# Optimization experiments

Measured on AMD Instinct MI355X. Metric: run time of the kernel, lower is better.

Reference implementation:

```python
import jax, jax.numpy as jnp
import numpy as np

H, HKV, DH, T_MAX = 32, 8, 128, 4096
ROPE_BASE = 500000.0


def apply_rope(x, pos, base):
    # x: [B, h, T, D]; MLX rope, traditional=False (split-half rotation)
    B, h, T, D = x.shape
    half = D // 2
    inv_freq = 1.0 / (base ** (jnp.arange(half, dtype=jnp.float32) * 2.0 / D))
    t = (pos + jnp.arange(T)).astype(jnp.float32)  # absolute positions
    ang = t[:, None] * inv_freq[None, :]           # [T, half]
    cos = jnp.cos(ang)[None, None]                 # [1,1,T,half]
    sin = jnp.sin(ang)[None, None]
    x1, x2 = x[..., :half], x[..., half:]
    return jnp.concatenate([x1 * cos - x2 * sin, x2 * cos + x1 * sin], axis=-1)


def setup_inputs() -> dict:
    key = jax.random.key(0)
    ks = jax.random.split(key, 5)
    hidden = 4096
    return {
        "hidden_states": jax.random.normal(ks[0], (1, 2048, hidden), jnp.float32),
        "Wq": jax.random.normal(ks[1], (hidden, H * DH), jnp.float32) * 0.02,
        "Wk": jax.random.normal(ks[2], (hidden, HKV * DH), jnp.float32) * 0.02,
        "Wv": jax.random.normal(ks[3], (hidden, HKV * DH), jnp.float32) * 0.02,
        "Wo": jax.random.normal(ks[4], (H * DH, hidden), jnp.float32) * 0.02,
        "pos_int": 0,
    }


def reference(hidden_states, Wq, Wk, Wv, Wo, pos_int):
    B, T, _ = hidden_states.shape
    q = (hidden_states @ Wq).reshape(B, T, H, DH).transpose(0, 2, 1, 3)    # [B,H,T,D]
    k = (hidden_states @ Wk).reshape(B, T, HKV, DH).transpose(0, 2, 1, 3)  # [B,Hkv,T,D]
    v = (hidden_states @ Wv).reshape(B, T, HKV, DH).transpose(0, 2, 1, 3)

    q = apply_rope(q, pos_int, ROPE_BASE)
    k = apply_rope(k, pos_int, ROPE_BASE)

    # KV cache: write at [pos:pos+T], then slice [:pos+T] (pos is static Python int)
    k_cache = jnp.zeros((B, HKV, T_MAX, DH), jnp.float32)
    v_cache = jnp.zeros((B, HKV, T_MAX, DH), jnp.float32)
    k_cache = jax.lax.dynamic_update_slice(k_cache, k, (0, 0, pos_int, 0))
    v_cache = jax.lax.dynamic_update_slice(v_cache, v, (0, 0, pos_int, 0))
    end_pos = pos_int + T
    k_ = k_cache[:, :, :end_pos, :]  # [B,Hkv,S,D]
    v_ = v_cache[:, :, :end_pos, :]
    S = end_pos

    # GQA without materializing repeat_interleave: group query heads per kv head
    group = H // HKV
    qg = q.reshape(B, HKV, group, T, DH)
    scale = 1.0 / jnp.sqrt(jnp.float32(DH))
    scores = jnp.einsum("bhgtd,bhsd->bhgts", qg, k_) * scale  # [B,Hkv,g,T,S]
    # torch SDPA is_causal=True: top-left aligned mask (allow s <= t)
    causal = jnp.arange(S)[None, :] <= jnp.arange(T)[:, None]  # [T,S]
    scores = jnp.where(causal[None, None, None], scores, -jnp.inf)
    probs = jax.nn.softmax(scores, axis=-1)
    attn = jnp.einsum("bhgts,bhsd->bhgtd", probs, v_)          # [B,Hkv,g,T,D]
    attn = attn.reshape(B, H, T, DH).transpose(0, 2, 1, 3).reshape(B, T, H * DH)
    return attn @ Wo
```

## Files before the change

kernel.cpp:

```cpp
#include <hip/hip_runtime.h>
#include <hip/hip_bf16.h>
#include <math.h>

typedef unsigned short u16;
typedef __attribute__((ext_vector_type(4))) float f32x4;
typedef __attribute__((ext_vector_type(8))) short bf16x8;

#define GLD16(gptr, lptr) __builtin_amdgcn_global_load_lds( \
    (const __attribute__((address_space(1))) void*)(gptr),  \
    (__attribute__((address_space(3))) void*)(lptr), 16, 0, 0)

__device__ __forceinline__ float bf2f(u16 u) {
  union { unsigned int i; float f; } c; c.i = ((unsigned int)u) << 16; return c.f;
}
__device__ __forceinline__ u16 f2bf(float f) {
  union { float f; unsigned int i; } c; c.f = f;
  unsigned int r = c.i + 0x7fffu + ((c.i >> 16) & 1u);
  return (u16)(r >> 16);
}

__global__ __launch_bounds__(256) void f32_to_bf16(const float* __restrict__ in,
                                                   u16* __restrict__ out, int n4) {
  int i = blockIdx.x * 256 + threadIdx.x;
  if (i >= n4) return;
  float4 v = reinterpret_cast<const float4*>(in)[i];
  ushort4 o;
  o.x = f2bf(v.x); o.y = f2bf(v.y); o.z = f2bf(v.z); o.w = f2bf(v.w);
  reinterpret_cast<ushort4*>(out)[i] = o;
}

__global__ __launch_bounds__(256) void transpose_qkv_w(const float* __restrict__ Wq,
                                                       const float* __restrict__ Wk,
                                                       const float* __restrict__ Wv,
                                                       u16* __restrict__ WT) {
  __shared__ float tile[32][33];
  const int bx = blockIdx.x, k0 = blockIdx.y * 32;
  const float* W; int n0, N; size_t outbase;
  if (bx < 128)      { W = Wq; n0 = bx * 32;          N = 4096; outbase = 0; }
  else if (bx < 160) { W = Wk; n0 = (bx - 128) * 32;  N = 1024; outbase = (size_t)4096 * 4096; }
  else               { W = Wv; n0 = (bx - 160) * 32;  N = 1024; outbase = (size_t)5120 * 4096; }
  const int tx = threadIdx.x & 31, ty = threadIdx.x >> 5;
#pragma unroll
  for (int r = 0; r < 32; r += 8)
    tile[ty + r][tx] = W[(size_t)(k0 + ty + r) * N + (n0 + tx)];
  __syncthreads();
#pragma unroll
  for (int r = 0; r < 32; r += 8)
    WT[outbase + (size_t)(n0 + ty + r) * 4096 + (k0 + tx)] = f2bf(tile[tx][ty + r]);
}

__global__ __launch_bounds__(256) void transpose_convert(const float* __restrict__ W,
                                                         u16* __restrict__ Wt,
                                                         int K, int N) {
  __shared__ float tile[32][33];
  const int n0 = blockIdx.x * 32, k0 = blockIdx.y * 32;
  const int tx = threadIdx.x & 31, ty = threadIdx.x >> 5;
#pragma unroll
  for (int r = 0; r < 32; r += 8)
    tile[ty + r][tx] = W[(size_t)(k0 + ty + r) * N + (n0 + tx)];
  __syncthreads();
#pragma unroll
  for (int r = 0; r < 32; r += 8)
    Wt[(size_t)(n0 + ty + r) * K + (k0 + tx)] = f2bf(tile[tx][ty + r]);
}

__global__ __launch_bounds__(256) void transpose_v(const u16* __restrict__ Vsrc,
                                                   u16* __restrict__ Vt) {
  __shared__ u16 tile[32][33];
  const int t0 = blockIdx.x * 32, d0 = blockIdx.y * 32, hkv = blockIdx.z;
  const int tx = threadIdx.x & 31, ty = threadIdx.x >> 5;
#pragma unroll
  for (int r = 0; r < 32; r += 8)
    tile[ty + r][tx] = Vsrc[(size_t)(t0 + ty + r) * 6144 + hkv * 128 + d0 + tx];
  __syncthreads();
#pragma unroll
  for (int r = 0; r < 32; r += 8)
    Vt[((size_t)hkv * 128 + d0 + ty + r) * 2048 + t0 + tx] = tile[tx][ty + r];
}

__global__ __launch_bounds__(256) void rope_table(float2* __restrict__ tab,
                                                  const int* __restrict__ pos_ptr) {
  int idx = blockIdx.x * 256 + threadIdx.x;
  int d = idx & 63, t = idx >> 6;
  int pos = *pos_ptr;
  float inv = exp2f(-(float)d * (0.015625f * 18.931568569324174f));
  float ang = (float)(pos + t) * inv;
  tab[idx] = make_float2(cosf(ang), sinf(ang));
}

__global__ __launch_bounds__(256) void rope_apply_qk(u16* __restrict__ QKV,
                                                     const float2* __restrict__ tab) {
  int idx = blockIdx.x * 256 + threadIdx.x;
  if (idx >= 2048 * 40 * 64) return;
  int d = idx & 63;
  int hh = (idx >> 6) % 40;
  int t = idx / (64 * 40);
  float2 cs = tab[t * 64 + d];
  const int col = (hh < 32) ? hh * 128 : 4096 + (hh - 32) * 128;
  size_t base = (size_t)t * 6144 + col + d;
  float x1 = bf2f(QKV[base]);
  float x2 = bf2f(QKV[base + 64]);
  QKV[base]      = f2bf(x1 * cs.x - x2 * cs.y);
  QKV[base + 64] = f2bf(x2 * cs.x + x1 * cs.y);
}

template <int BN, int OUT_BF16>
__global__ __launch_bounds__(512, 4) void gemm_2cu(const u16* __restrict__ A,
                                                   const u16* __restrict__ Bt,
                                                   void* __restrict__ C,
                                                   int M, int N, int K) {
  constexpr int NF = BN / 64;
  constexpr int WCOL = BN / 4;
  constexpr int LB = BN / 64;
  __shared__ alignas(16) u16 As[2][128 * 64];
  __shared__ alignas(16) u16 Bs[2][BN * 64];
  const int tid = threadIdx.x;
  const int lane = tid & 63, wid = tid >> 6;
  const int l15 = lane & 15, lg = lane >> 4;
  const int wm = wid >> 2, wn = wid & 3;
  const int wvb = tid & ~63;

  const int gy = gridDim.y;
  const int id0 = blockIdx.y * gridDim.x + blockIdx.x;
  const int xcd = id0 & 7;
  const int l = id0 >> 3;
  const int m0 = (l % gy) * 128;
  const int n0 = (xcd * (gridDim.x >> 3) + l / gy) * BN;

  f32x4 acc[4][NF];
#pragma unroll
  for (int i = 0; i < 4; ++i)
#pragma unroll
    for (int j = 0; j < NF; ++j) {
      f32x4 zz = {0.f, 0.f, 0.f, 0.f};
      acc[i][j] = zz;
    }

#define STAGE(s_, b_)                                                           \
  do {                                                                          \
    _Pragma("unroll")                                                           \
    for (int p = 0; p < 2; ++p) {                                               \
      const int slot = p * 512 + tid;                                           \
      const int row = slot >> 3, ch = slot & 7;                                 \
      const int col = (ch ^ (row & 7)) * 8;                                     \
      GLD16(A + (size_t)(m0 + row) * K + (s_) * 64 + col,                       \
            &As[b_][(p * 512 + wvb) * 8]);                                      \
    }                                                                           \
    _Pragma("unroll")                                                           \
    for (int p = 0; p < LB; ++p) {                                              \
      const int slot = p * 512 + tid;                                           \
      const int row = slot >> 3, ch = slot & 7;                                 \
      const int col = (ch ^ (row & 7)) * 8;                                     \
      GLD16(Bt + (size_t)(n0 + row) * K + (s_) * 64 + col,                      \
            &Bs[b_][(p * 512 + wvb) * 8]);                                      \
    }                                                                           \
  } while (0)

  STAGE(0, 0);
  __syncthreads();
  int cur = 0;

  const int nt = K >> 6;
  for (int t = 0; t < nt; ++t) {
    if (t + 1 < nt) STAGE(t + 1, cur ^ 1);
#pragma unroll
    for (int g = 0; g < 2; ++g) {
      bf16x8 af[4], bfr[NF];
#pragma unroll
      for (int i = 0; i < 4; ++i) {
        const int row = wm * 64 + i * 16 + l15;
        const int ch = (g * 4 + lg) ^ (row & 7);
        af[i] = *reinterpret_cast<const bf16x8*>(&As[cur][row * 64 + ch * 8]);
      }
#pragma unroll
      for (int j = 0; j < NF; ++j) {
        const int row = wn * WCOL + j * 16 + l15;
        const int ch = (g * 4 + lg) ^ (row & 7);
        bfr[j] = *reinterpret_cast<const bf16x8*>(&Bs[cur][row * 64 + ch * 8]);
      }
      __builtin_amdgcn_s_setprio(1);
#pragma unroll
      for (int i = 0; i < 4; ++i)
#pragma unroll
        for (int j = 0; j < NF; ++j)
          acc[i][j] = __builtin_amdgcn_mfma_f32_16x16x32_bf16(af[i], bfr[j], acc[i][j], 0, 0, 0);
      __builtin_amdgcn_s_setprio(0);
    }
    __syncthreads();
    cur ^= 1;
  }
#undef STAGE

#pragma unroll
  for (int i = 0; i < 4; ++i)
#pragma unroll
    for (int j = 0; j < NF; ++j)
#pragma unroll
      for (int r = 0; r < 4; ++r) {
        const int row = m0 + wm * 64 + i * 16 + lg * 4 + r;
        const int col = n0 + wn * WCOL + j * 16 + l15;
        const float v = acc[i][j][r];
        if (OUT_BF16) ((u16*)C)[(size_t)row * N + col] = f2bf(v);
        else          ((float*)C)[(size_t)row * N + col] = v;
      }
}

__global__ __launch_bounds__(512) void attn_kernel(const u16* __restrict__ Q,
                                                   const u16* __restrict__ K,
                                                   const u16* __restrict__ Vt,
                                                   u16* __restrict__ O,
                                                   const int* __restrict__ pos_ptr) {
  const int pos = *pos_ptr;
  const int id = (int)(blockIdx.y * gridDim.x + blockIdx.x);
  const int hkv = id & 7;
  const int h = hkv * 4 + ((id >> 3) & 3);
  const int qp = id >> 5;
  const int tid = threadIdx.x;
  const int w = tid >> 6, lane = tid & 63;
  const int l15 = lane & 15, lg = lane >> 4;

  __shared__ alignas(16) u16 Ks[2][64 * 128];
  __shared__ alignas(16) u16 Vs[2][128 * 64];
  __shared__ alignas(16) u16 Pl[8][16][72];

  const u16* Kh = K + hkv * 128;
  const u16* Vh = Vt + (size_t)hkv * 128 * 2048;

  const float C = 0.12752961957823275f;
  const float THR = 62.0f;
  const int wvb = tid & ~63;

#define STAGE_TILE(st_, b_)                                                        \
  do {                                                                             \
    const int s0_ = (st_) * 64;                                                    \
    _Pragma("unroll")                                                              \
    for (int p = 0; p < 2; ++p) {                                                  \
      const int idx = p * 512 + tid;                                               \
      const int kr = idx >> 4, kc = (idx & 15) ^ (kr & 7);                         \
      GLD16(Kh + (size_t)(s0_ + kr) * 6144 + kc * 8, &Ks[b_][(p * 512 + wvb) * 8]);\
      const int vr = idx >> 3, vc = (idx & 7) ^ (vr & 7);                          \
      GLD16(Vh + (size_t)vr * 2048 + s0_ + vc * 8, &Vs[b_][(p * 512 + wvb) * 8]);  \
    }                                                                              \
  } while (0)

  for (int pass = 0; pass < 2; ++pass) {
    const int qb = (pass == 0) ? (8 + qp) : (7 - qp);
    const int qt0 = qb * 128;
    const int nst = 2 * qb + 2;
    const int frag_base = qt0 + w * 16;

    bf16x8 qa[4];
#pragma unroll
    for (int kk = 0; kk < 4; ++kk)
      qa[kk] = *reinterpret_cast<const bf16x8*>(
          Q + (size_t)(frag_base + l15) * 6144 + h * 128 + kk * 32 + lg * 8);

    f32x4 acc[8];
#pragma unroll
    for (int i = 0; i < 8; ++i) { f32x4 z = {0.f, 0.f, 0.f, 0.f}; acc[i] = z; }
    float mrun[4], lpart[4];
#pragma unroll
    for (int r = 0; r < 4; ++r) {
      mrun[r] = (pos > 0) ? 0.0f : -INFINITY;
      lpart[r] = 0.0f;
    }

    STAGE_TILE(0, 0);
    __syncthreads();
    int cur = 0;

    for (int st = 0; st < nst; ++st) {
      if (st + 1 < nst) STAGE_TILE(st + 1, cur ^ 1);
      const int s0 = st * 64;

      float pv[4][4];
      __builtin_amdgcn_s_setprio(1);
#pragma unroll
      for (int sub = 0; sub < 4; ++sub) {
        f32x4 s4 = {0.f, 0.f, 0.f, 0.f};
        const int row = sub * 16 + l15;
#pragma unroll
        for (int kk = 0; kk < 4; ++kk) {
          const int chunk = (kk * 4 + lg) ^ (row & 7);
          bf16x8 kf = *reinterpret_cast<const bf16x8*>(&Ks[cur][row * 128 + chunk * 8]);
          s4 = __builtin_amdgcn_mfma_f32_16x16x32_bf16(qa[kk], kf, s4, 0, 0, 0);
        }
#pragma unroll
        for (int r = 0; r < 4; ++r) pv[sub][r] = s4[r];
      }
      __builtin_amdgcn_s_setprio(0);

      if (s0 + 64 > frag_base) {
#pragma unroll
        for (int r = 0; r < 4; ++r) {
          const int qrow = frag_base + lg * 4 + r;
#pragma unroll
          for (int sub = 0; sub < 4; ++sub) {
            const int scol = s0 + sub * 16 + l15;
            pv[sub][r] = (scol <= qrow) ? pv[sub][r] : -INFINITY;
          }
        }
      }

      float lmax[4];
#pragma unroll
      for (int r = 0; r < 4; ++r)
        lmax[r] = fmaxf(fmaxf(pv[0][r], pv[1][r]), fmaxf(pv[2][r], pv[3][r]));
      float dml = fmaxf(fmaxf(lmax[0] - mrun[0], lmax[1] - mrun[1]),
                        fmaxf(lmax[2] - mrun[2], lmax[3] - mrun[3]));
      if (!__all(dml <= THR)) {
        float sfr[4];
#pragma unroll
        for (int r = 0; r < 4; ++r) {
          float mx = lmax[r];
#pragma unroll
          for (int off = 1; off < 16; off <<= 1) mx = fmaxf(mx, __shfl_xor(mx, off));
          const float mnew = fmaxf(mrun[r], mx);
          sfr[r] = exp2f((mrun[r] - mnew) * C);
          mrun[r] = mnew;
          lpart[r] *= sfr[r];
        }
#pragma unroll
        for (int dc = 0; dc < 8; ++dc)
#pragma unroll
          for (int r = 0; r < 4; ++r) acc[dc][r] *= sfr[r];
      }

#pragma unroll
      for (int r = 0; r < 4; ++r) {
        const float nmC = -mrun[r] * C;
        float ps = 0.0f;
#pragma unroll
        for (int sub = 0; sub < 4; ++sub) {
          const float p = exp2f(fmaf(pv[sub][r], C, nmC));
          pv[sub][r] = p;
          ps += p;
        }
        lpart[r] += ps;
      }

#pragma unroll
      for (int sub = 0; sub < 4; ++sub)
#pragma unroll
        for (int r = 0; r < 4; ++r)
          Pl[w][lg * 4 + r][sub * 16 + l15] = f2bf(pv[sub][r]);

      __builtin_amdgcn_s_setprio(1);
#pragma unroll
      for (int ks = 0; ks < 2; ++ks) {
        bf16x8 pf = *reinterpret_cast<const bf16x8*>(&Pl[w][l15][ks * 32 + lg * 8]);
#pragma unroll
        for (int dc = 0; dc < 8; ++dc) {
          const int row = dc * 16 + l15;
          const int chunk = (ks * 4 + lg) ^ (row & 7);
          bf16x8 vf = *reinterpret_cast<const bf16x8*>(&Vs[cur][row * 64 + chunk * 8]);
          acc[dc] = __builtin_amdgcn_mfma_f32_16x16x32_bf16(pf, vf, acc[dc], 0, 0, 0);
        }
      }
      __builtin_amdgcn_s_setprio(0);

      __syncthreads();
      cur ^= 1;
    }

#pragma unroll
    for (int r = 0; r < 4; ++r) {
      float l = lpart[r];
#pragma unroll
      for (int off = 1; off < 16; off <<= 1) l += __shfl_xor(l, off);
      if (pos > 0) l += (float)pos * exp2f(-mrun[r] * C);
      const float linv = 1.0f / l;
      const int qrow = frag_base + lg * 4 + r;
#pragma unroll
      for (int dc = 0; dc < 8; ++dc)
        O[(size_t)qrow * 4096 + h * 128 + dc * 16 + l15] = f2bf(acc[dc][r] * linv);
    }
  }
#undef STAGE_TILE
}

extern "C" void kernel_launch(void* const* d_in, const int* in_sizes, int n_in,
                              void* d_out, int out_size, void* d_ws, size_t ws_size,
                              hipStream_t stream) {
  const float* hs = (const float*)d_in[0];
  const float* Wq = (const float*)d_in[1];
  const float* Wk = (const float*)d_in[2];
  const float* Wv = (const float*)d_in[3];
  const float* Wo = (const float*)d_in[4];
  const int* pos  = (const int*)d_in[5];

  char* ws = (char*)d_ws;
  u16* hs_bf = (u16*)(ws + 0);
  u16* WT    = (u16*)(ws + 16777216ULL);
  u16* QKVb  = (u16*)(ws + 67108864ULL);
  u16* attnO = hs_bf;
  u16* WoT   = WT;
  u16* Vtg   = (u16*)(ws + 50331648ULL);
  float2* tabF = (float2*)(ws + 54525952ULL);

  f32_to_bf16<<<8192, 256, 0, stream>>>(hs, hs_bf, 2097152);
  transpose_qkv_w<<<dim3(192, 128), 256, 0, stream>>>(Wq, Wk, Wv, WT);

  gemm_2cu<192, 1><<<dim3(32, 16), 512, 0, stream>>>(hs_bf, WT, QKVb, 2048, 6144, 4096);

  transpose_convert<<<dim3(128, 128), 256, 0, stream>>>(Wo, WoT, 4096, 4096);

  rope_table<<<512, 256, 0, stream>>>(tabF, pos);
  rope_apply_qk<<<20480, 256, 0, stream>>>(QKVb, tabF);

  transpose_v<<<dim3(64, 4, 8), 256, 0, stream>>>(QKVb + 5120, Vtg);

  attn_kernel<<<dim3(8, 32), 512, 0, stream>>>(QKVb, QKVb + 4096, Vtg, attnO, pos);

  gemm_2cu<128, 0><<<dim3(32, 16), 512, 0, stream>>>(attnO, WoT, d_out, 2048, 4096, 4096);
}
```

Baseline: 342.0 us.

## Split attention into one block per query tile with occupancy hint and halved P staging

Before, each attention block handled two paired query tiles in sequence (256 blocks). Now each block handles a single 128-row query tile (512 blocks), with the longest causal tiles dispatched first. The launch bounds ask for 4 blocks per CU, and the P matrix goes through LDS in two 32-column halves, which shrinks the Pl buffer. This aims at better load balance and occupancy on the many-CU device, at the cost of more blocks reloading their Q fragments and extra per-block setup, and the occupancy hint may force register spilling.

```diff
diff --git a/kernel.cpp b/kernel.cpp
--- a/kernel.cpp
+++ b/kernel.cpp
@@ -205,23 +205,24 @@
       }
 }
 
-__global__ __launch_bounds__(512) void attn_kernel(const u16* __restrict__ Q,
-                                                   const u16* __restrict__ K,
-                                                   const u16* __restrict__ Vt,
-                                                   u16* __restrict__ O,
-                                                   const int* __restrict__ pos_ptr) {
+__global__ __launch_bounds__(512, 4) void attn_kernel(const u16* __restrict__ Q,
+                                                      const u16* __restrict__ K,
+                                                      const u16* __restrict__ Vt,
+                                                      u16* __restrict__ O,
+                                                      const int* __restrict__ pos_ptr) {
   const int pos = *pos_ptr;
-  const int id = (int)(blockIdx.y * gridDim.x + blockIdx.x);
-  const int hkv = id & 7;
-  const int h = hkv * 4 + ((id >> 3) & 3);
-  const int qp = id >> 5;
+  const int id = (int)blockIdx.x;
+  const int hq = id & 255;
+  const int h = hq >> 3;
+  const int qb = (id < 256) ? (15 - (hq & 7)) : (hq & 7);
+  const int hkv = h >> 2;
   const int tid = threadIdx.x;
   const int w = tid >> 6, lane = tid & 63;
   const int l15 = lane & 15, lg = lane >> 4;
 
   __shared__ alignas(16) u16 Ks[2][64 * 128];
   __shared__ alignas(16) u16 Vs[2][128 * 64];
-  __shared__ alignas(16) u16 Pl[8][16][72];
+  __shared__ alignas(16) u16 Pl[8][16][40];
 
   const u16* Kh = K + hkv * 128;
   const u16* Vh = Vt + (size_t)hkv * 128 * 2048;
@@ -243,138 +244,134 @@
     }                                                                              \
   } while (0)
 
-  for (int pass = 0; pass < 2; ++pass) {
-    const int qb = (pass == 0) ? (8 + qp) : (7 - qp);
-    const int qt0 = qb * 128;
-    const int nst = 2 * qb + 2;
-    const int frag_base = qt0 + w * 16;
-
-    bf16x8 qa[4];
-#pragma unroll
-    for (int kk = 0; kk < 4; ++kk)
-      qa[kk] = *reinterpret_cast<const bf16x8*>(
-          Q + (size_t)(frag_base + l15) * 6144 + h * 128 + kk * 32 + lg * 8);
-
-    f32x4 acc[8];
-#pragma unroll
-    for (int i = 0; i < 8; ++i) { f32x4 z = {0.f, 0.f, 0.f, 0.f}; acc[i] = z; }
-    float mrun[4], lpart[4];
-#pragma unroll
-    for (int r = 0; r < 4; ++r) {
-      mrun[r] = (pos > 0) ? 0.0f : -INFINITY;
-      lpart[r] = 0.0f;
-    }
-
-    STAGE_TILE(0, 0);
-    __syncthreads();
-    int cur = 0;
-
-    for (int st = 0; st < nst; ++st) {
-      if (st + 1 < nst) STAGE_TILE(st + 1, cur ^ 1);
-      const int s0 = st * 64;
-
-      float pv[4][4];
-      __builtin_amdgcn_s_setprio(1);
-#pragma unroll
-      for (int sub = 0; sub < 4; ++sub) {
-        f32x4 s4 = {0.f, 0.f, 0.f, 0.f};
-        const int row = sub * 16 + l15;
-#pragma unroll
-        for (int kk = 0; kk < 4; ++kk) {
-          const int chunk = (kk * 4 + lg) ^ (row & 7);
-          bf16x8 kf = *reinterpret_cast<const bf16x8*>(&Ks[cur][row * 128 + chunk * 8]);
-          s4 = __builtin_amdgcn_mfma_f32_16x16x32_bf16(qa[kk], kf, s4, 0, 0, 0);
+  const int qt0 = qb * 128;
+  const int nst = 2 * qb + 2;
+  const int frag_base = qt0 + w * 16;
+
+  bf16x8 qa[4];
+#pragma unroll
+  for (int kk = 0; kk < 4; ++kk)
+    qa[kk] = *reinterpret_cast<const bf16x8*>(
+        Q + (size_t)(frag_base + l15) * 6144 + h * 128 + kk * 32 + lg * 8);
+
+  f32x4 acc[8];
+#pragma unroll
+  for (int i = 0; i < 8; ++i) { f32x4 z = {0.f, 0.f, 0.f, 0.f}; acc[i] = z; }
+  float mrun[4], lpart[4];
+#pragma unroll
+  for (int r = 0; r < 4; ++r) {
+    mrun[r] = (pos > 0) ? 0.0f : -INFINITY;
+    lpart[r] = 0.0f;
+  }
+
+  STAGE_TILE(0, 0);
+  __syncthreads();
+  int cur = 0;
+
+  for (int st = 0; st < nst; ++st) {
+    if (st + 1 < nst) STAGE_TILE(st + 1, cur ^ 1);
+    const int s0 = st * 64;
+
+    float pv[4][4];
+    __builtin_amdgcn_s_setprio(1);
+#pragma unroll
+    for (int sub = 0; sub < 4; ++sub) {
+      f32x4 s4 = {0.f, 0.f, 0.f, 0.f};
+      const int row = sub * 16 + l15;
+#pragma unroll
+      for (int kk = 0; kk < 4; ++kk) {
+        const int chunk = (kk * 4 + lg) ^ (row & 7);
+        bf16x8 kf = *reinterpret_cast<const bf16x8*>(&Ks[cur][row * 128 + chunk * 8]);
+        s4 = __builtin_amdgcn_mfma_f32_16x16x32_bf16(qa[kk], kf, s4, 0, 0, 0);
+      }
+#pragma unroll
+      for (int r = 0; r < 4; ++r) pv[sub][r] = s4[r];
+    }
+    __builtin_amdgcn_s_setprio(0);
+
+    if (s0 + 64 > frag_base) {
+#pragma unroll
+      for (int r = 0; r < 4; ++r) {
+        const int qrow = frag_base + lg * 4 + r;
+#pragma unroll
+        for (int sub = 0; sub < 4; ++sub) {
+          const int scol = s0 + sub * 16 + l15;
+          pv[sub][r] = (scol <= qrow) ? pv[sub][r] : -INFINITY;
         }
-#pragma unroll
-        for (int r = 0; r < 4; ++r) pv[sub][r] = s4[r];
-      }
-      __builtin_amdgcn_s_setprio(0);
-
-      if (s0 + 64 > frag_base) {
-#pragma unroll
-        for (int r = 0; r < 4; ++r) {
-          const int qrow = frag_base + lg * 4 + r;
-#pragma unroll
-          for (int sub = 0; sub < 4; ++sub) {
-            const int scol = s0 + sub * 16 + l15;
-            pv[sub][r] = (scol <= qrow) ? pv[sub][r] : -INFINITY;
-          }
-        }
-      }
-
-      float lmax[4];
-#pragma unroll
-      for (int r = 0; r < 4; ++r)
-        lmax[r] = fmaxf(fmaxf(pv[0][r], pv[1][r]), fmaxf(pv[2][r], pv[3][r]));
-      float dml = fmaxf(fmaxf(lmax[0] - mrun[0], lmax[1] - mrun[1]),
-                        fmaxf(lmax[2] - mrun[2], lmax[3] - mrun[3]));
-      if (!__all(dml <= THR)) {
-        float sfr[4];
-#pragma unroll
-        for (int r = 0; r < 4; ++r) {
-          float mx = lmax[r];
-#pragma unroll
-          for (int off = 1; off < 16; off <<= 1) mx = fmaxf(mx, __shfl_xor(mx, off));
-          const float mnew = fmaxf(mrun[r], mx);
-          sfr[r] = exp2f((mrun[r] - mnew) * C);
-          mrun[r] = mnew;
-          lpart[r] *= sfr[r];
-        }
-#pragma unroll
-        for (int dc = 0; dc < 8; ++dc)
-#pragma unroll
-          for (int r = 0; r < 4; ++r) acc[dc][r] *= sfr[r];
-      }
-
+      }
+    }
+
+    float dml = -INFINITY;
+#pragma unroll
+    for (int r = 0; r < 4; ++r)
+      dml = fmaxf(dml, fmaxf(fmaxf(pv[0][r], pv[1][r]),
+                             fmaxf(pv[2][r], pv[3][r])) - mrun[r]);
+    if (!__all(dml <= THR)) {
+      float sfr[4];
+#pragma unroll
+      for (int r = 0; r < 4; ++r) {
+        float mx = fmaxf(fmaxf(pv[0][r], pv[1][r]), fmaxf(pv[2][r], pv[3][r]));
+#pragma unroll
+        for (int off = 1; off < 16; off <<= 1) mx = fmaxf(mx, __shfl_xor(mx, off));
+        const float mnew = fmaxf(mrun[r], mx);
+        sfr[r] = exp2f((mrun[r] - mnew) * C);
+        mrun[r] = mnew;
+        lpart[r] *= sfr[r];
+      }
+#pragma unroll
+      for (int dc = 0; dc < 8; ++dc)
+#pragma unroll
+        for (int r = 0; r < 4; ++r) acc[dc][r] *= sfr[r];
+    }
+
+#pragma unroll
+    for (int half = 0; half < 2; ++half) {
 #pragma unroll
       for (int r = 0; r < 4; ++r) {
         const float nmC = -mrun[r] * C;
         float ps = 0.0f;
 #pragma unroll
-        for (int sub = 0; sub < 4; ++sub) {
+        for (int s2 = 0; s2 < 2; ++s2) {
+          const int sub = half * 2 + s2;
           const float p = exp2f(fmaf(pv[sub][r], C, nmC));
           pv[sub][r] = p;
           ps += p;
         }
         lpart[r] += ps;
       }
-
-#pragma unroll
-      for (int sub = 0; sub < 4; ++sub)
+#pragma unroll
+      for (int s2 = 0; s2 < 2; ++s2)
 #pragma unroll
         for (int r = 0; r < 4; ++r)
-          Pl[w][lg * 4 + r][sub * 16 + l15] = f2bf(pv[sub][r]);
-
+          Pl[w][lg * 4 + r][s2 * 16 + l15] = f2bf(pv[half * 2 + s2][r]);
+
+      bf16x8 pf = *reinterpret_cast<const bf16x8*>(&Pl[w][l15][lg * 8]);
       __builtin_amdgcn_s_setprio(1);
 #pragma unroll
-      for (int ks = 0; ks < 2; ++ks) {
-        bf16x8 pf = *reinterpret_cast<const bf16x8*>(&Pl[w][l15][ks * 32 + lg * 8]);
-#pragma unroll
-        for (int dc = 0; dc < 8; ++dc) {
-          const int row = dc * 16 + l15;
-          const int chunk = (ks * 4 + lg) ^ (row & 7);
-          bf16x8 vf = *reinterpret_cast<const bf16x8*>(&Vs[cur][row * 64 + chunk * 8]);
-          acc[dc] = __builtin_amdgcn_mfma_f32_16x16x32_bf16(pf, vf, acc[dc], 0, 0, 0);
-        }
+      for (int dc = 0; dc < 8; ++dc) {
+        const int row = dc * 16 + l15;
+        const int chunk = (half * 4 + lg) ^ (row & 7);
+        bf16x8 vf = *reinterpret_cast<const bf16x8*>(&Vs[cur][row * 64 + chunk * 8]);
+        acc[dc] = __builtin_amdgcn_mfma_f32_16x16x32_bf16(pf, vf, acc[dc], 0, 0, 0);
       }
       __builtin_amdgcn_s_setprio(0);
-
-      __syncthreads();
-      cur ^= 1;
-    }
-
-#pragma unroll
-    for (int r = 0; r < 4; ++r) {
-      float l = lpart[r];
-#pragma unroll
-      for (int off = 1; off < 16; off <<= 1) l += __shfl_xor(l, off);
-      if (pos > 0) l += (float)pos * exp2f(-mrun[r] * C);
-      const float linv = 1.0f / l;
-      const int qrow = frag_base + lg * 4 + r;
-#pragma unroll
-      for (int dc = 0; dc < 8; ++dc)
-        O[(size_t)qrow * 4096 + h * 128 + dc * 16 + l15] = f2bf(acc[dc][r] * linv);
-    }
+    }
+
+    __syncthreads();
+    cur ^= 1;
+  }
+
+#pragma unroll
+  for (int r = 0; r < 4; ++r) {
+    float l = lpart[r];
+#pragma unroll
+    for (int off = 1; off < 16; off <<= 1) l += __shfl_xor(l, off);
+    if (pos > 0) l += (float)pos * exp2f(-mrun[r] * C);
+    const float linv = 1.0f / l;
+    const int qrow = frag_base + lg * 4 + r;
+#pragma unroll
+    for (int dc = 0; dc < 8; ++dc)
+      O[(size_t)qrow * 4096 + h * 128 + dc * 16 + l15] = f2bf(acc[dc][r] * linv);
   }
 #undef STAGE_TILE
 }
@@ -410,7 +407,7 @@
 
   transpose_v<<<dim3(64, 4, 8), 256, 0, stream>>>(QKVb + 5120, Vtg);
 
-  attn_kernel<<<dim3(8, 32), 512, 0, stream>>>(QKVb, QKVb + 4096, Vtg, attnO, pos);
+  attn_kernel<<<dim3(512), 512, 0, stream>>>(QKVb, QKVb + 4096, Vtg, attnO, pos);
 
   gemm_2cu<128, 0><<<dim3(32, 16), 512, 0, stream>>>(attnO, WoT, d_out, 2048, 4096, 4096);
 }
```

After: 331.9 us. -2.9%, faster.
